# Kernel optimization log

Measured on AMD Instinct MI355X. Metric: run time of the kernel, lower is better.

## Reference

```python
import jax, jax.numpy as jnp
import numpy as np

LN_EPS = 1e-5

def setup_inputs() -> dict:
    key = jax.random.key(0)
    k1, k2, k3, k4 = jax.random.split(key, 4)
    B, N, F, O = 8, 2048, 256, 256
    x = jax.random.normal(k1, (B, N, F), dtype=jnp.float32)
    adj = jax.random.uniform(k2, (B, N, N), dtype=jnp.float32)
    # LayerNorm affine params
    gamma = jnp.ones((F,), jnp.float32)
    beta = jnp.zeros((F,), jnp.float32)
    # Linear weights stored as [in, out] (torch stores [out, in]; math identical)
    W_self = jax.random.normal(k3, (F, O), dtype=jnp.float32) * (1.0 / np.sqrt(F))
    W_neigh = jax.random.normal(k4, (F, O), dtype=jnp.float32) * (1.0 / np.sqrt(F))
    return {"x": x, "adj": adj, "gamma": gamma, "beta": beta,
            "W_self": W_self, "W_neigh": W_neigh}

def reference(x, adj, gamma, beta, W_self, W_neigh):
    # LayerNorm over last dim
    mu = jnp.mean(x, axis=-1, keepdims=True)
    var = jnp.mean(jnp.square(x - mu), axis=-1, keepdims=True)
    xn = (x - mu) * jax.lax.rsqrt(var + LN_EPS) * gamma + beta

    # Normalized Laplacian: I - D_out^{-1/2} A D_in^{-1/2}
    # out_degree = column sums (dim=1), in_degree = row sums (dim=2)
    d_out = jnp.sum(adj, axis=1)   # [B, N]
    d_in = jnp.sum(adj, axis=2)    # [B, N]
    s_out = jnp.where(d_out != 0, jax.lax.rsqrt(d_out), 0.0)
    s_in = jnp.where(d_in != 0, jax.lax.rsqrt(d_in), 0.0)
    # diag(s_out) @ A @ diag(s_in) == row/col elementwise rescale (no N^3 work)
    A_norm = s_out[:, :, None] * adj * s_in[:, None, :]
    eye = jnp.eye(adj.shape[1], dtype=adj.dtype)
    L = eye[None, :, :] - A_norm    # [B, N, N]

    neighbor = jnp.einsum('bij,bjf->bif', L, xn)   # [B, N, F]
    pre = xn @ W_self + neighbor @ W_neigh          # [B, N, O]
    return jax.nn.softplus(pre)
```

## Files before the change

kernel.cpp:

```cpp
#include <hip/hip_runtime.h>
#include <stdint.h>

#define B_ 8
#define N_ 2048
#define F_ 256

typedef unsigned short u16;
typedef __attribute__((ext_vector_type(8))) short bf16x8;
typedef __attribute__((ext_vector_type(4))) float f32x4;

__device__ __forceinline__ u16 f2bf(float f) {
    uint32_t u = __builtin_bit_cast(uint32_t, f);
    u += 0x7FFFu + ((u >> 16) & 1u);
    return (u16)(u >> 16);
}
__device__ __forceinline__ uint32_t pack2(float a, float b) {
    return (uint32_t)f2bf(a) | ((uint32_t)f2bf(b) << 16);
}

__device__ __forceinline__ void gload_lds16(const void* g, void* lds_uniform_base) {
    __builtin_amdgcn_global_load_lds(
        (const __attribute__((address_space(1))) uint32_t*)g,
        (__attribute__((address_space(3))) uint32_t*)lds_uniform_base, 16, 0, 0);
}

__global__ __launch_bounds__(256) void k_adj(const float* __restrict__ adj,
                                             u16* __restrict__ adj_bf,
                                             float* __restrict__ pcol,
                                             float* __restrict__ prow) {
    const int panel = blockIdx.x, half = blockIdx.y, b = blockIdx.z;
    const int t = threadIdx.x, w = t >> 6, l = t & 63;
    const float* base = adj + ((size_t)b * N_ + (size_t)panel * 16) * N_ + half * 1024;
    u16* abf = adj_bf + ((size_t)b * N_ + (size_t)panel * 16) * N_ + half * 1024;
    float c[4];
#pragma unroll
    for (int e = 0; e < 4; ++e) c[e] = 0.f;
    __shared__ float rs[16][4];
#pragma unroll 4
    for (int r = 0; r < 16; ++r) {
        const float4 v = *(const float4*)(base + (size_t)r * N_ + t * 4);
        c[0] += v.x; c[1] += v.y; c[2] += v.z; c[3] += v.w;
        *(uint2*)&abf[(size_t)r * N_ + t * 4] = make_uint2(pack2(v.x, v.y), pack2(v.z, v.w));
        float s = (v.x + v.y) + (v.z + v.w);
#pragma unroll
        for (int off = 32; off; off >>= 1) s += __shfl_xor(s, off);
        if (l == 0) rs[r][w] = s;
    }
    float4* pc = (float4*)(pcol + ((size_t)(b * 128 + panel)) * N_ + half * 1024);
    pc[t] = make_float4(c[0], c[1], c[2], c[3]);
    __syncthreads();
    if (t < 16)
        prow[(size_t)half * (B_ * N_) + (size_t)b * N_ + panel * 16 + t]
            = rs[t][0] + rs[t][1] + rs[t][2] + rs[t][3];
}

__global__ __launch_bounds__(256) void k_mid(const float* __restrict__ x,
                                             const float* __restrict__ gamma,
                                             const float* __restrict__ beta,
                                             const float* __restrict__ prow,
                                             const float* __restrict__ pcol,
                                             const float* __restrict__ Ws,
                                             const float* __restrict__ Wn,
                                             u16* __restrict__ xn,
                                             u16* __restrict__ yT,
                                             float* __restrict__ deg_col,
                                             u16* __restrict__ WcT,
                                             u16* __restrict__ WnT) {
    const int bx = blockIdx.x;
    const int t = threadIdx.x;
    __shared__ u16 yt[256 * 34];
    if (bx < 512) {
        const int b = bx >> 6, panel = bx & 63;
        const int w = t >> 6, l = t & 63;
        float g[4], be[4];
#pragma unroll
        for (int m = 0; m < 4; ++m) { g[m] = gamma[l + 64 * m]; be[m] = beta[l + 64 * m]; }
        for (int rr = 0; rr < 8; ++rr) {
            const int jj = w * 8 + rr;
            const int j = panel * 32 + jj;
            const float rowsum = prow[(size_t)b * N_ + j] + prow[(size_t)(B_ * N_) + (size_t)b * N_ + j];
            const float sin_ = (rowsum != 0.f) ? rsqrtf(rowsum) : 0.f;
            const float* xp = x + ((size_t)b * N_ + j) * F_;
            float v[4], s = 0.f, ss = 0.f;
#pragma unroll
            for (int m = 0; m < 4; ++m) { v[m] = xp[l + 64 * m]; s += v[m]; ss += v[m] * v[m]; }
#pragma unroll
            for (int off = 32; off; off >>= 1) { s += __shfl_xor(s, off); ss += __shfl_xor(ss, off); }
            const float mu = s * (1.f / 256.f);
            const float var = ss * (1.f / 256.f) - mu * mu;
            const float rstd = rsqrtf(var + 1e-5f);
            u16* xnp = xn + ((size_t)b * N_ + j) * F_;
#pragma unroll
            for (int m = 0; m < 4; ++m) {
                const float xv = (v[m] - mu) * rstd * g[m] + be[m];
                xnp[l + 64 * m] = f2bf(xv);
                yt[(l + 64 * m) * 34 + jj] = f2bf(sin_ * xv);
            }
        }
        __syncthreads();
#pragma unroll
        for (int m2 = 0; m2 < 2; ++m2) {
            const int f = (t >> 1) + 128 * m2;
            const int jj0 = (t & 1) * 16;
            uint32_t vals[8];
#pragma unroll
            for (int e = 0; e < 8; ++e) vals[e] = *(const uint32_t*)&yt[f * 34 + jj0 + 2 * e];
            uint4* dst = (uint4*)(yT + ((size_t)b * F_ + f) * N_ + panel * 32 + jj0);
            dst[0] = make_uint4(vals[0], vals[1], vals[2], vals[3]);
            dst[1] = make_uint4(vals[4], vals[5], vals[6], vals[7]);
        }
    } else if (bx < 576) {
        const int tid = (bx - 512) * 256 + t;
        const int b = tid >> 11, j = tid & 2047;
        const float* p = pcol + (size_t)b * 128 * N_ + j;
        float s = 0.f;
#pragma unroll 8
        for (int g = 0; g < 128; ++g) s += p[(size_t)g * N_];
        deg_col[tid] = s;
    } else {
        const int rel = bx - 576;
#pragma unroll 4
        for (int e = 0; e < 32; ++e) {
            const int idx = rel * 8192 + e * 256 + t;
            const int k = idx >> 8, o = idx & 255;
            const float a = Ws[idx], q = Wn[idx];
            WcT[o * 256 + k] = f2bf(a + q);
            WnT[o * 256 + k] = f2bf(-q);
        }
    }
}

__global__ __launch_bounds__(256) void k_gemm1(const u16* __restrict__ adj_bf,
                                               const u16* __restrict__ yT,
                                               const float* __restrict__ deg_col,
                                               u16* __restrict__ z) {
    const int blk = blockIdx.x;
    const int b = blk & 7;
    const int kk = blk >> 3;
    const int nt = kk & 1;
    const int m = kk >> 1;
    const int i0 = m * 64, f0 = nt * 128;
    const int t = threadIdx.x, w = t >> 6, l = t & 63;
    const int wr = w >> 1, wc = w & 1;
    alignas(16) __shared__ u16 As[64 * 32];
    alignas(16) __shared__ u16 Bs[128 * 32];
    f32x4 acc[2][4];
#pragma unroll
    for (int mi = 0; mi < 2; ++mi)
#pragma unroll
        for (int ni = 0; ni < 4; ++ni) acc[mi][ni] = (f32x4)0.f;

    const u16* abase = adj_bf + ((size_t)b * N_ + i0) * N_;
    const u16* ybase = yT + ((size_t)b * F_ + f0) * (size_t)N_;
    const int lr = l >> 2, lb = (l & 3) * 16;

    for (int kt = 0; kt < 64; ++kt) {
        const int k0b = kt * 64;
        gload_lds16((const char*)(abase + (size_t)(w * 16 + lr) * N_) + k0b + lb,
                    (char*)As + (w << 10));
#pragma unroll
        for (int q = 0; q < 2; ++q)
            gload_lds16((const char*)(ybase + (size_t)(q * 64 + w * 16 + lr) * N_) + k0b + lb,
                        (char*)Bs + q * 4096 + (w << 10));
        __syncthreads();
        bf16x8 af[2], bfr[4];
#pragma unroll
        for (int mi = 0; mi < 2; ++mi)
            af[mi] = *(const bf16x8*)&As[(wr * 32 + mi * 16 + (l & 15)) * 32 + (l >> 4) * 8];
#pragma unroll
        for (int ni = 0; ni < 4; ++ni)
            bfr[ni] = *(const bf16x8*)&Bs[(wc * 64 + ni * 16 + (l & 15)) * 32 + (l >> 4) * 8];
#pragma unroll
        for (int mi = 0; mi < 2; ++mi)
#pragma unroll
            for (int ni = 0; ni < 4; ++ni)
                acc[mi][ni] = __builtin_amdgcn_mfma_f32_16x16x32_bf16(af[mi], bfr[ni], acc[mi][ni], 0, 0, 0);
        __syncthreads();
    }
#pragma unroll
    for (int mi = 0; mi < 2; ++mi) {
#pragma unroll
        for (int r = 0; r < 4; ++r) {
            const int row = i0 + wr * 32 + mi * 16 + (l >> 4) * 4 + r;
            const float d = deg_col[(size_t)b * N_ + row];
            const float so = (d != 0.f) ? rsqrtf(d) : 0.f;
#pragma unroll
            for (int ni = 0; ni < 4; ++ni) {
                const int col = f0 + wc * 64 + ni * 16 + (l & 15);
                z[((size_t)b * N_ + row) * F_ + col] = f2bf(so * acc[mi][ni][r]);
            }
        }
    }
}

__global__ __launch_bounds__(256) void k_gemm2(const u16* __restrict__ xn,
                                               const u16* __restrict__ z,
                                               const u16* __restrict__ WcT,
                                               const u16* __restrict__ WnT,
                                               float* __restrict__ out) {
    const int blk = blockIdx.x;
    const int xcd = blk & 7;
    const int kk = blk >> 3;
    const int nt = kk & 1;
    const int mt = xcd + 8 * (kk >> 1);
    const int r0 = mt * 64, o0 = nt * 128;
    const int t = threadIdx.x, w = t >> 6, l = t & 63;
    const int wr = w >> 1, wc = w & 1;
    alignas(16) __shared__ u16 As[64 * 32];
    alignas(16) __shared__ u16 Bs[128 * 32];
    f32x4 acc[2][4];
#pragma unroll
    for (int mi = 0; mi < 2; ++mi)
#pragma unroll
        for (int ni = 0; ni < 4; ++ni) acc[mi][ni] = (f32x4)0.f;

    const int lr = l >> 2, lb = (l & 3) * 16;

    for (int kt = 0; kt < 16; ++kt) {
        const u16* asrc = (kt < 8) ? xn : z;
        const u16* bsrc = (kt < 8) ? WcT : WnT;
        const int kk0b = (kt & 7) * 64;
        gload_lds16((const char*)(asrc + (size_t)(r0 + w * 16 + lr) * F_) + kk0b + lb,
                    (char*)As + (w << 10));
#pragma unroll
        for (int q = 0; q < 2; ++q)
            gload_lds16((const char*)(bsrc + (size_t)(o0 + q * 64 + w * 16 + lr) * F_) + kk0b + lb,
                        (char*)Bs + q * 4096 + (w << 10));
        __syncthreads();
        bf16x8 af[2], bfr[4];
#pragma unroll
        for (int mi = 0; mi < 2; ++mi)
            af[mi] = *(const bf16x8*)&As[(wr * 32 + mi * 16 + (l & 15)) * 32 + (l >> 4) * 8];
#pragma unroll
        for (int ni = 0; ni < 4; ++ni)
            bfr[ni] = *(const bf16x8*)&Bs[(wc * 64 + ni * 16 + (l & 15)) * 32 + (l >> 4) * 8];
#pragma unroll
        for (int mi = 0; mi < 2; ++mi)
#pragma unroll
            for (int ni = 0; ni < 4; ++ni)
                acc[mi][ni] = __builtin_amdgcn_mfma_f32_16x16x32_bf16(af[mi], bfr[ni], acc[mi][ni], 0, 0, 0);
        __syncthreads();
    }
#pragma unroll
    for (int mi = 0; mi < 2; ++mi) {
#pragma unroll
        for (int r = 0; r < 4; ++r) {
            const int rr = r0 + wr * 32 + mi * 16 + (l >> 4) * 4 + r;
#pragma unroll
            for (int ni = 0; ni < 4; ++ni) {
                const int cc = o0 + wc * 64 + ni * 16 + (l & 15);
                const float p = acc[mi][ni][r];
                out[(size_t)rr * F_ + cc] = (p > 20.f) ? p : log1pf(expf(p));
            }
        }
    }
}

extern "C" void kernel_launch(void* const* d_in, const int* in_sizes, int n_in,
                              void* d_out, int out_size, void* d_ws, size_t ws_size,
                              hipStream_t stream) {
    (void)in_sizes; (void)n_in; (void)out_size; (void)ws_size;
    const float* x     = (const float*)d_in[0];
    const float* adj   = (const float*)d_in[1];
    const float* gamma = (const float*)d_in[2];
    const float* beta  = (const float*)d_in[3];
    const float* Ws    = (const float*)d_in[4];
    const float* Wn    = (const float*)d_in[5];
    float* out = (float*)d_out;

    char* ws = (char*)d_ws;
    float* deg_col = (float*)(ws + 0);
    float* prow    = (float*)(ws + 65536);
    u16* xn     = (u16*)(ws + 196608);
    u16* yT     = (u16*)(ws + 8585216);
    u16* z      = (u16*)(ws + 16973824);
    u16* WcT    = (u16*)(ws + 25362432);
    u16* WnT    = (u16*)(ws + 25493504);
    u16* adj_bf = (u16*)(ws + 25624576);
    float* pcol = (float*)z;

    k_adj  <<<dim3(128, 2, 8), 256, 0, stream>>>(adj, adj_bf, pcol, prow);
    k_mid  <<<584, 256, 0, stream>>>(x, gamma, beta, prow, pcol, Ws, Wn,
                                     xn, yT, deg_col, WcT, WnT);
    k_gemm1<<<512, 256, 0, stream>>>(adj_bf, yT, deg_col, z);
    k_gemm2<<<512, 256, 0, stream>>>(xn, z, WcT, WnT, out);
}
```

Baseline: 304.3 us.

## Double-buffer LDS tiles in both GEMMs, enlarge gemm1 tile, batch adj loads

Both GEMM kernels now double-buffer their LDS tiles: the next K-slice is issued with global_load_lds before the current slice's MFMAs, and one barrier per iteration replaces two. k_gemm1 switches to 128x128 tiles with 512 threads and 256 blocks, which halves how often the yT operand is re-read. k_adj loads four rows before processing them, to raise memory-level parallelism. The risks are fewer resident blocks per CU from the larger LDS footprint and block size, and only 256 blocks to cover all CUs in gemm1.

```diff
diff --git a/kernel.cpp b/kernel.cpp
--- a/kernel.cpp
+++ b/kernel.cpp
@@ -36,15 +36,22 @@
 #pragma unroll
     for (int e = 0; e < 4; ++e) c[e] = 0.f;
     __shared__ float rs[16][4];
-#pragma unroll 4
-    for (int r = 0; r < 16; ++r) {
-        const float4 v = *(const float4*)(base + (size_t)r * N_ + t * 4);
-        c[0] += v.x; c[1] += v.y; c[2] += v.z; c[3] += v.w;
-        *(uint2*)&abf[(size_t)r * N_ + t * 4] = make_uint2(pack2(v.x, v.y), pack2(v.z, v.w));
-        float s = (v.x + v.y) + (v.z + v.w);
-#pragma unroll
-        for (int off = 32; off; off >>= 1) s += __shfl_xor(s, off);
-        if (l == 0) rs[r][w] = s;
+#pragma unroll
+    for (int rb = 0; rb < 16; rb += 4) {
+        float4 v[4];
+#pragma unroll
+        for (int q = 0; q < 4; ++q)
+            v[q] = *(const float4*)(base + (size_t)(rb + q) * N_ + t * 4);
+#pragma unroll
+        for (int q = 0; q < 4; ++q) {
+            c[0] += v[q].x; c[1] += v[q].y; c[2] += v[q].z; c[3] += v[q].w;
+            *(uint2*)&abf[(size_t)(rb + q) * N_ + t * 4] =
+                make_uint2(pack2(v[q].x, v[q].y), pack2(v[q].z, v[q].w));
+            float s = (v[q].x + v[q].y) + (v[q].z + v[q].w);
+#pragma unroll
+            for (int off = 32; off; off >>= 1) s += __shfl_xor(s, off);
+            if (l == 0) rs[rb + q][w] = s;
+        }
     }
     float4* pc = (float4*)(pcol + ((size_t)(b * 128 + panel)) * N_ + half * 1024);
     pc[t] = make_float4(c[0], c[1], c[2], c[3]);
@@ -130,7 +137,7 @@
     }
 }
 
-__global__ __launch_bounds__(256) void k_gemm1(const u16* __restrict__ adj_bf,
+__global__ __launch_bounds__(512) void k_gemm1(const u16* __restrict__ adj_bf,
                                                const u16* __restrict__ yT,
                                                const float* __restrict__ deg_col,
                                                u16* __restrict__ z) {
@@ -139,55 +146,60 @@
     const int kk = blk >> 3;
     const int nt = kk & 1;
     const int m = kk >> 1;
-    const int i0 = m * 64, f0 = nt * 128;
+    const int i0 = m * 128, f0 = nt * 128;
     const int t = threadIdx.x, w = t >> 6, l = t & 63;
-    const int wr = w >> 1, wc = w & 1;
-    alignas(16) __shared__ u16 As[64 * 32];
-    alignas(16) __shared__ u16 Bs[128 * 32];
-    f32x4 acc[2][4];
-#pragma unroll
-    for (int mi = 0; mi < 2; ++mi)
-#pragma unroll
-        for (int ni = 0; ni < 4; ++ni) acc[mi][ni] = (f32x4)0.f;
+    const int wr = w >> 2, wc = w & 3;
+    alignas(16) __shared__ u16 As[2][128 * 32];
+    alignas(16) __shared__ u16 Bs[2][128 * 32];
+    f32x4 acc[4][2];
+#pragma unroll
+    for (int mi = 0; mi < 4; ++mi)
+#pragma unroll
+        for (int ni = 0; ni < 2; ++ni) acc[mi][ni] = (f32x4)0.f;
 
     const u16* abase = adj_bf + ((size_t)b * N_ + i0) * N_;
     const u16* ybase = yT + ((size_t)b * F_ + f0) * (size_t)N_;
-    const int lr = l >> 2, lb = (l & 3) * 16;
+    const int o = w * 1024 + l * 16;
+    const int row = o >> 6, kb = o & 63;
+
+    gload_lds16((const char*)(abase + (size_t)row * N_) + kb, (char*)&As[0][0] + (w << 10));
+    gload_lds16((const char*)(ybase + (size_t)row * N_) + kb, (char*)&Bs[0][0] + (w << 10));
+    __syncthreads();
 
     for (int kt = 0; kt < 64; ++kt) {
-        const int k0b = kt * 64;
-        gload_lds16((const char*)(abase + (size_t)(w * 16 + lr) * N_) + k0b + lb,
-                    (char*)As + (w << 10));
-#pragma unroll
-        for (int q = 0; q < 2; ++q)
-            gload_lds16((const char*)(ybase + (size_t)(q * 64 + w * 16 + lr) * N_) + k0b + lb,
-                        (char*)Bs + q * 4096 + (w << 10));
-        __syncthreads();
-        bf16x8 af[2], bfr[4];
-#pragma unroll
-        for (int mi = 0; mi < 2; ++mi)
-            af[mi] = *(const bf16x8*)&As[(wr * 32 + mi * 16 + (l & 15)) * 32 + (l >> 4) * 8];
-#pragma unroll
-        for (int ni = 0; ni < 4; ++ni)
-            bfr[ni] = *(const bf16x8*)&Bs[(wc * 64 + ni * 16 + (l & 15)) * 32 + (l >> 4) * 8];
-#pragma unroll
-        for (int mi = 0; mi < 2; ++mi)
-#pragma unroll
-            for (int ni = 0; ni < 4; ++ni)
+        const int cb = kt & 1, nb = cb ^ 1;
+        if (kt < 63) {
+            const int knb = (kt + 1) * 64;
+            gload_lds16((const char*)(abase + (size_t)row * N_) + knb + kb,
+                        (char*)&As[nb][0] + (w << 10));
+            gload_lds16((const char*)(ybase + (size_t)row * N_) + knb + kb,
+                        (char*)&Bs[nb][0] + (w << 10));
+        }
+        bf16x8 af[4], bfr[2];
+#pragma unroll
+        for (int mi = 0; mi < 4; ++mi)
+            af[mi] = *(const bf16x8*)&As[cb][(wr * 64 + mi * 16 + (l & 15)) * 32 + (l >> 4) * 8];
+#pragma unroll
+        for (int ni = 0; ni < 2; ++ni)
+            bfr[ni] = *(const bf16x8*)&Bs[cb][(wc * 32 + ni * 16 + (l & 15)) * 32 + (l >> 4) * 8];
+#pragma unroll
+        for (int mi = 0; mi < 4; ++mi)
+#pragma unroll
+            for (int ni = 0; ni < 2; ++ni)
                 acc[mi][ni] = __builtin_amdgcn_mfma_f32_16x16x32_bf16(af[mi], bfr[ni], acc[mi][ni], 0, 0, 0);
         __syncthreads();
     }
 #pragma unroll
-    for (int mi = 0; mi < 2; ++mi) {
+    for (int mi = 0; mi < 4; ++mi) {
 #pragma unroll
         for (int r = 0; r < 4; ++r) {
-            const int row = i0 + wr * 32 + mi * 16 + (l >> 4) * 4 + r;
-            const float d = deg_col[(size_t)b * N_ + row];
+            const int rowz = i0 + wr * 64 + mi * 16 + (l >> 4) * 4 + r;
+            const float d = deg_col[(size_t)b * N_ + rowz];
             const float so = (d != 0.f) ? rsqrtf(d) : 0.f;
 #pragma unroll
-            for (int ni = 0; ni < 4; ++ni) {
-                const int col = f0 + wc * 64 + ni * 16 + (l & 15);
-                z[((size_t)b * N_ + row) * F_ + col] = f2bf(so * acc[mi][ni][r]);
+            for (int ni = 0; ni < 2; ++ni) {
+                const int col = f0 + wc * 32 + ni * 16 + (l & 15);
+                z[((size_t)b * N_ + rowz) * F_ + col] = f2bf(so * acc[mi][ni][r]);
             }
         }
     }
@@ -206,34 +218,45 @@
     const int r0 = mt * 64, o0 = nt * 128;
     const int t = threadIdx.x, w = t >> 6, l = t & 63;
     const int wr = w >> 1, wc = w & 1;
-    alignas(16) __shared__ u16 As[64 * 32];
-    alignas(16) __shared__ u16 Bs[128 * 32];
+    alignas(16) __shared__ u16 As[2][64 * 32];
+    alignas(16) __shared__ u16 Bs[2][128 * 32];
     f32x4 acc[2][4];
 #pragma unroll
     for (int mi = 0; mi < 2; ++mi)
 #pragma unroll
         for (int ni = 0; ni < 4; ++ni) acc[mi][ni] = (f32x4)0.f;
 
-    const int lr = l >> 2, lb = (l & 3) * 16;
+    const int o = w * 1024 + l * 16;
+    const int arow = o >> 6, kb = o & 63;
+
+    gload_lds16((const char*)(xn + (size_t)(r0 + arow) * F_) + kb, (char*)&As[0][0] + (w << 10));
+#pragma unroll
+    for (int q = 0; q < 2; ++q)
+        gload_lds16((const char*)(WcT + (size_t)(o0 + q * 64 + arow) * F_) + kb,
+                    (char*)&Bs[0][0] + q * 4096 + (w << 10));
+    __syncthreads();
 
     for (int kt = 0; kt < 16; ++kt) {
-        const u16* asrc = (kt < 8) ? xn : z;
-        const u16* bsrc = (kt < 8) ? WcT : WnT;
-        const int kk0b = (kt & 7) * 64;
-        gload_lds16((const char*)(asrc + (size_t)(r0 + w * 16 + lr) * F_) + kk0b + lb,
-                    (char*)As + (w << 10));
-#pragma unroll
-        for (int q = 0; q < 2; ++q)
-            gload_lds16((const char*)(bsrc + (size_t)(o0 + q * 64 + w * 16 + lr) * F_) + kk0b + lb,
-                        (char*)Bs + q * 4096 + (w << 10));
-        __syncthreads();
+        const int cb = kt & 1, nb = cb ^ 1;
+        if (kt < 15) {
+            const int kn = kt + 1;
+            const u16* asrc = (kn < 8) ? xn : z;
+            const u16* bsrc = (kn < 8) ? WcT : WnT;
+            const int knb = (kn & 7) * 64;
+            gload_lds16((const char*)(asrc + (size_t)(r0 + arow) * F_) + knb + kb,
+                        (char*)&As[nb][0] + (w << 10));
+#pragma unroll
+            for (int q = 0; q < 2; ++q)
+                gload_lds16((const char*)(bsrc + (size_t)(o0 + q * 64 + arow) * F_) + knb + kb,
+                            (char*)&Bs[nb][0] + q * 4096 + (w << 10));
+        }
         bf16x8 af[2], bfr[4];
 #pragma unroll
         for (int mi = 0; mi < 2; ++mi)
-            af[mi] = *(const bf16x8*)&As[(wr * 32 + mi * 16 + (l & 15)) * 32 + (l >> 4) * 8];
+            af[mi] = *(const bf16x8*)&As[cb][(wr * 32 + mi * 16 + (l & 15)) * 32 + (l >> 4) * 8];
 #pragma unroll
         for (int ni = 0; ni < 4; ++ni)
-            bfr[ni] = *(const bf16x8*)&Bs[(wc * 64 + ni * 16 + (l & 15)) * 32 + (l >> 4) * 8];
+            bfr[ni] = *(const bf16x8*)&Bs[cb][(wc * 64 + ni * 16 + (l & 15)) * 32 + (l >> 4) * 8];
 #pragma unroll
         for (int mi = 0; mi < 2; ++mi)
 #pragma unroll
@@ -282,6 +305,6 @@
     k_adj  <<<dim3(128, 2, 8), 256, 0, stream>>>(adj, adj_bf, pcol, prow);
     k_mid  <<<584, 256, 0, stream>>>(x, gamma, beta, prow, pcol, Ws, Wn,
                                      xn, yT, deg_col, WcT, WnT);
-    k_gemm1<<<512, 256, 0, stream>>>(adj_bf, yT, deg_col, z);
+    k_gemm1<<<256, 512, 0, stream>>>(adj_bf, yT, deg_col, z);
     k_gemm2<<<512, 256, 0, stream>>>(xn, z, WcT, WnT, out);
 }
```

New measurement: 315.7 us. 1.04x slower.
